# Kernel optimization log

Measured on AMD Instinct MI355X. Metric: run time of the kernel, lower is better.

The kernel has to match this reference:

```python
import jax, jax.numpy as jnp
import numpy as np

N_NODES = 50000
N_EDGES = 800000
IN_F = 128
HID = 128
OUT = 2


def setup_inputs() -> dict:
    key = jax.random.key(0)
    ks = jax.random.split(key, 10)
    x = jax.random.normal(ks[0], (N_NODES, IN_F), dtype=jnp.float32)
    edge_index = jax.random.randint(ks[1], (2, N_EDGES), 0, N_NODES, dtype=jnp.int64)

    def lin(k, fan_in, fan_out):
        s = 1.0 / np.sqrt(fan_in)
        return jax.random.uniform(k, (fan_in, fan_out), jnp.float32, -s, s)

    return {
        "x": x,
        "edge_index": edge_index,
        # SAGEConv1: lin_l applied to mean-aggregated neighbors (with bias),
        # lin_r applied to root features (no bias), PyG convention.
        "W1_l": lin(ks[2], IN_F, HID),
        "W1_r": lin(ks[3], IN_F, HID),
        "b1": jnp.zeros((HID,), jnp.float32),
        "W2_l": lin(ks[4], HID, HID),
        "W2_r": lin(ks[5], HID, HID),
        "b2": jnp.zeros((HID,), jnp.float32),
        "Wfc": lin(ks[6], HID, OUT),
        "bfc": jnp.zeros((OUT,), jnp.float32),
    }


def reference(x, edge_index, W1_l, W1_r, b1, W2_l, W2_r, b2, Wfc, bfc):
    n = x.shape[0]
    src = edge_index[0]  # message source j
    dst = edge_index[1]  # aggregation target i
    # in-degree for mean aggregation (clamp to avoid div-by-zero for isolated nodes)
    deg = jax.ops.segment_sum(jnp.ones_like(dst, dtype=x.dtype), dst, num_segments=n)
    inv_deg = 1.0 / jnp.maximum(deg, 1.0)  # [n]

    def sage_conv(h, Wl, Wr, b):
        # mean over incoming neighbor features, then two linear maps
        agg = jax.ops.segment_sum(h[src], dst, num_segments=n) * inv_deg[:, None]
        return agg @ Wl + h @ Wr + b

    # dropout is identity at inference (training=False)
    h = jax.nn.relu(sage_conv(x, W1_l, W1_r, b1))
    h = jax.nn.relu(sage_conv(h, W2_l, W2_r, b2))
    return h @ Wfc + bfc  # [n, out] logits
```

## Files before the change

### kernel.cpp

```cpp
#include <hip/hip_runtime.h>

#define NN 50000
#define NE 800000
#define NBLK_S ((NE + 255) / 256)
#define DEGCAP 64

#define CVT_BLKS 6250
#define PREP_BLKS 32
#define ZERO_BLKS 50
#define SETUP_GRID (CVT_BLKS + PREP_BLKS + ZERO_BLKS)

typedef short short8 __attribute__((ext_vector_type(8)));
typedef short short4v __attribute__((ext_vector_type(4)));
typedef float f32x4 __attribute__((ext_vector_type(4)));
typedef _Float16 half8v __attribute__((ext_vector_type(8)));

__device__ inline unsigned short f16_bits(float f) {
    _Float16 h = (_Float16)f;
    return __builtin_bit_cast(unsigned short, h);
}

__global__ __launch_bounds__(256) void setup_kernel(const float* __restrict__ x,
                                                    unsigned short* __restrict__ xb,
                                                    const float* __restrict__ W0,
                                                    const float* __restrict__ W1,
                                                    const float* __restrict__ W2,
                                                    const float* __restrict__ W3,
                                                    short* __restrict__ wf,
                                                    int* __restrict__ deg,
                                                    unsigned short* __restrict__ h1b) {
    int b = blockIdx.x;
    if (b < CVT_BLKS) {
        int i = b * 256 + threadIdx.x;
        float4 v = ((const float4*)x)[i];
        short4v r;
        r[0] = (short)f16_bits(v.x);
        r[1] = (short)f16_bits(v.y);
        r[2] = (short)f16_bits(v.z);
        r[3] = (short)f16_bits(v.w);
        ((short4v*)xb)[i] = r;
    } else if (b < CVT_BLKS + PREP_BLKS) {
        int t = (b - CVT_BLKS) * 256 + threadIdx.x;
        int mat = t >> 11;
        const float* W = (mat == 0) ? W0 : (mat == 1) ? W1 : (mat == 2) ? W2 : W3;
        short* out = wf + (size_t)mat * 16384;
        int r = t & 2047;
        int nt = r >> 8;
        int kc = (r >> 6) & 3;
        int lane = r & 63;
        int n = nt * 16 + (lane & 15);
        int kbase = kc * 32 + ((lane >> 4) << 3);
        short8 vh;
#pragma unroll
        for (int j = 0; j < 8; ++j) {
            float w = W[(size_t)(kbase + j) * 128 + n];
            vh[j] = (short)f16_bits(w);
        }
        size_t o = ((size_t)((nt * 4 + kc) * 64 + lane)) * 8;
        *(short8*)(out + o) = vh;
    } else {
        int bl = b - CVT_BLKS - PREP_BLKS;
        int idx = bl * 256 + threadIdx.x;
        if (idx < (NN / 4)) ((int4*)deg)[idx] = make_int4(0, 0, 0, 0);
        if (bl == ZERO_BLKS - 1) {
            int t = threadIdx.x;
            short8 z = {0, 0, 0, 0, 0, 0, 0, 0};
            if (t < 16) *(short8*)(xb + ((size_t)NN << 7) + (t << 3)) = z;
            else if (t < 32) *(short8*)(h1b + ((size_t)NN << 7) + ((t - 16) << 3)) = z;
        }
    }
}

__global__ __launch_bounds__(256) void scatter_kernel(const int* __restrict__ src,
                                                      const int* __restrict__ dst,
                                                      int* __restrict__ deg,
                                                      int* __restrict__ col, int ne) {
    int i = blockIdx.x * 256 + threadIdx.x;
    if (i >= ne) return;
    int d = dst[i];
    int s = src[i];
    int slot = atomicAdd(&deg[d], 1);
    col[((size_t)d << 6) + slot] = s;
}

__global__ __launch_bounds__(256) void agg_kernel(const unsigned short* __restrict__ hb,
                                                  const int* __restrict__ col,
                                                  const int* __restrict__ deg,
                                                  unsigned short* __restrict__ outb, int n) {
    int node = blockIdx.x * 4 + (threadIdx.x >> 6);
    if (node >= n) return;
    int lane = threadIdx.x & 63;
    int slot = lane >> 4, sub = lane & 15;
    int dg = deg[node];
    const unsigned short* base = hb + (sub << 3);
    const int* cp = col + ((size_t)node << 6);
    float acc[8];
#pragma unroll
    for (int j = 0; j < 8; ++j) acc[j] = 0.f;

    for (int e0 = slot; e0 < dg; e0 += 16) {
        int c[4];
#pragma unroll
        for (int j = 0; j < 4; ++j) {
            int e = e0 + 4 * j;
            int cc = cp[e < DEGCAP ? e : 0];
            c[j] = (e < dg) ? cc : NN;
        }
        half8v v[4];
#pragma unroll
        for (int j = 0; j < 4; ++j) v[j] = *(const half8v*)(base + ((size_t)c[j] << 7));
        half8v s = (v[0] + v[1]) + (v[2] + v[3]);
#pragma unroll
        for (int q = 0; q < 8; ++q) acc[q] += (float)s[q];
    }
#pragma unroll
    for (int j = 0; j < 8; ++j) {
        acc[j] += __shfl_xor(acc[j], 16, 64);
        acc[j] += __shfl_xor(acc[j], 32, 64);
    }
    if (slot == 0) {
        float s = 1.0f / (float)(dg > 0 ? dg : 1);
        short8 o;
#pragma unroll
        for (int j = 0; j < 8; ++j) o[j] = (short)f16_bits(acc[j] * s);
        *(short8*)(outb + ((size_t)node << 7) + (sub << 3)) = o;
    }
}

__global__ __launch_bounds__(256) void gemm_mfma(const unsigned short* __restrict__ A0b,
                                                 const unsigned short* __restrict__ A1b,
                                                 const short* __restrict__ Wf0,
                                                 const short* __restrict__ Wf1,
                                                 const float* __restrict__ bias,
                                                 unsigned short* __restrict__ outb,
                                                 const float* __restrict__ Wfc,
                                                 const float* __restrict__ bfc,
                                                 float* __restrict__ fcout,
                                                 int n, int relu) {
    int lane = threadIdx.x & 63;
    int wave = threadIdx.x >> 6;
    int quad = lane >> 4, m16 = lane & 15;
    int row_base = blockIdx.x * 64 + wave * 16;
    int arow = row_base + m16;
    if (arow > n - 1) arow = n - 1;

    const unsigned short* ap0 = A0b + ((size_t)arow << 7) + (quad << 3);
    const unsigned short* ap1 = A1b + ((size_t)arow << 7) + (quad << 3);
    half8v a0[4], a1[4];
#pragma unroll
    for (int kc = 0; kc < 4; ++kc) {
        a0[kc] = *(const half8v*)(ap0 + kc * 32);
        a1[kc] = *(const half8v*)(ap1 + kc * 32);
    }

    f32x4 acc[8];
#pragma unroll
    for (int nt = 0; nt < 8; ++nt) acc[nt] = (f32x4){0.f, 0.f, 0.f, 0.f};

#pragma unroll
    for (int kc = 0; kc < 4; ++kc) {
        const short* wp0 = Wf0 + ((size_t)kc * 64 + lane) * 8;
        const short* wp1 = Wf1 + ((size_t)kc * 64 + lane) * 8;
#pragma unroll
        for (int nt = 0; nt < 8; ++nt) {
            half8v b0 = *(const half8v*)(wp0 + (size_t)nt * 2048);
            half8v b1 = *(const half8v*)(wp1 + (size_t)nt * 2048);
            acc[nt] = __builtin_amdgcn_mfma_f32_16x16x32_f16(a0[kc], b0, acc[nt], 0, 0, 0);
            acc[nt] = __builtin_amdgcn_mfma_f32_16x16x32_f16(a1[kc], b1, acc[nt], 0, 0, 0);
        }
    }

    float bcol[8];
#pragma unroll
    for (int nt = 0; nt < 8; ++nt) bcol[nt] = bias[nt * 16 + m16];

    if (Wfc) {
        float w0[8], w1[8];
#pragma unroll
        for (int nt = 0; nt < 8; ++nt) {
            float2 wv = *(const float2*)(Wfc + 2 * (nt * 16 + m16));
            w0[nt] = wv.x;
            w1[nt] = wv.y;
        }
        float b0 = bfc[0], b1 = bfc[1];
#pragma unroll
        for (int r = 0; r < 4; ++r) {
            float p0 = 0.f, p1 = 0.f;
#pragma unroll
            for (int nt = 0; nt < 8; ++nt) {
                float v = fmaxf(acc[nt][r] + bcol[nt], 0.f);
                p0 += v * w0[nt];
                p1 += v * w1[nt];
            }
#pragma unroll
            for (int off = 1; off < 16; off <<= 1) {
                p0 += __shfl_xor(p0, off, 64);
                p1 += __shfl_xor(p1, off, 64);
            }
            int row = row_base + quad * 4 + r;
            if (m16 == 0 && row < n) {
                float2 o;
                o.x = p0 + b0;
                o.y = p1 + b1;
                *(float2*)(fcout + 2 * (size_t)row) = o;
            }
        }
    } else {
#pragma unroll
        for (int r = 0; r < 4; ++r) {
            int row = row_base + quad * 4 + r;
            if (row >= n) continue;
            unsigned short* opb = outb + ((size_t)row << 7) + m16;
#pragma unroll
            for (int nt = 0; nt < 8; ++nt) {
                float v = acc[nt][r] + bcol[nt];
                if (relu) v = fmaxf(v, 0.f);
                opb[nt * 16] = f16_bits(v);
            }
        }
    }
}

extern "C" void kernel_launch(void* const* d_in, const int* in_sizes, int n_in,
                              void* d_out, int out_size, void* d_ws, size_t ws_size,
                              hipStream_t stream) {
    const float* x   = (const float*)d_in[0];
    const int* edge  = (const int*)d_in[1];
    const float* W1l = (const float*)d_in[2];
    const float* W1r = (const float*)d_in[3];
    const float* b1  = (const float*)d_in[4];
    const float* W2l = (const float*)d_in[5];
    const float* W2r = (const float*)d_in[6];
    const float* b2  = (const float*)d_in[7];
    const float* Wfc = (const float*)d_in[8];
    const float* bfc = (const float*)d_in[9];
    float* out = (float*)d_out;

    const int n = NN, ne = NE;
    const int* src = edge;
    const int* dst = edge + ne;

    char* ws = (char*)d_ws;
    size_t off = 0;
    auto alloc = [&](size_t bytes) -> char* {
        char* p = ws + off;
        off = (off + bytes + 511) & ~(size_t)511;
        return p;
    };
    int* deg         = (int*)alloc((size_t)NN * 4);
    short* wf        = (short*)alloc((size_t)4 * 16384 * 2);
    int* col         = (int*)alloc((size_t)NN * DEGCAP * 4);
    unsigned short* xb   = (unsigned short*)alloc((size_t)(n + 1) * 128 * 2);
    unsigned short* aggb = (unsigned short*)alloc((size_t)n * 128 * 2);
    unsigned short* h1b  = (unsigned short*)alloc((size_t)(n + 1) * 128 * 2);
    (void)ws_size; (void)in_sizes; (void)n_in; (void)out_size;

    setup_kernel<<<SETUP_GRID, 256, 0, stream>>>(x, xb, W1l, W1r, W2l, W2r, wf, deg, h1b);
    scatter_kernel<<<NBLK_S, 256, 0, stream>>>(src, dst, deg, col, ne);

    agg_kernel<<<(n + 3) / 4, 256, 0, stream>>>(xb, col, deg, aggb, n);
    gemm_mfma<<<(n + 63) / 64, 256, 0, stream>>>(aggb, xb, wf, wf + 16384, b1, h1b,
                                                 (const float*)0, (const float*)0, (float*)0, n, 1);
    agg_kernel<<<(n + 3) / 4, 256, 0, stream>>>(h1b, col, deg, aggb, n);
    gemm_mfma<<<(n + 63) / 64, 256, 0, stream>>>(aggb, h1b, wf + 2 * 16384, wf + 3 * 16384, b2,
                                                 (unsigned short*)0, Wfc, bfc, out, n, 1);
}
```

Measured before the change: 230.1 us.

## Partition edge scatter by XCD destination range and store 16-bit neighbor indices

```diff
diff --git a/kernel.cpp b/kernel.cpp
--- a/kernel.cpp
+++ b/kernel.cpp
@@ -2,8 +2,13 @@
 
 #define NN 50000
 #define NE 800000
-#define NBLK_S ((NE + 255) / 256)
 #define DEGCAP 64
+
+#define NXCD 8
+#define NPS ((NN + NXCD - 1) / NXCD)
+#define SEPB 4096
+#define NCHUNK ((NE + SEPB - 1) / SEPB)
+#define SCAT_GRID (NCHUNK * NXCD)
 
 #define CVT_BLKS 6250
 #define PREP_BLKS 32
@@ -74,17 +79,25 @@
 __global__ __launch_bounds__(256) void scatter_kernel(const int* __restrict__ src,
                                                       const int* __restrict__ dst,
                                                       int* __restrict__ deg,
-                                                      int* __restrict__ col, int ne) {
-    int i = blockIdx.x * 256 + threadIdx.x;
-    if (i >= ne) return;
-    int d = dst[i];
-    int s = src[i];
-    int slot = atomicAdd(&deg[d], 1);
-    col[((size_t)d << 6) + slot] = s;
+                                                      unsigned short* __restrict__ col, int ne) {
+    int slot8 = blockIdx.x & 7;
+    int chunk = blockIdx.x >> 3;
+    int lo = slot8 * NPS, hi = lo + NPS;
+    int base = chunk * SEPB;
+    int end = base + SEPB;
+    if (end > ne) end = ne;
+    for (int i = base + threadIdx.x; i < end; i += 256) {
+        int d = dst[i];
+        if (d >= lo && d < hi) {
+            int s = src[i];
+            int sl = atomicAdd(&deg[d], 1);
+            col[((size_t)d << 6) + sl] = (unsigned short)s;
+        }
+    }
 }
 
 __global__ __launch_bounds__(256) void agg_kernel(const unsigned short* __restrict__ hb,
-                                                  const int* __restrict__ col,
+                                                  const unsigned short* __restrict__ col,
                                                   const int* __restrict__ deg,
                                                   unsigned short* __restrict__ outb, int n) {
     int node = blockIdx.x * 4 + (threadIdx.x >> 6);
@@ -93,7 +106,7 @@
     int slot = lane >> 4, sub = lane & 15;
     int dg = deg[node];
     const unsigned short* base = hb + (sub << 3);
-    const int* cp = col + ((size_t)node << 6);
+    const unsigned short* cp = col + ((size_t)node << 6);
     float acc[8];
 #pragma unroll
     for (int j = 0; j < 8; ++j) acc[j] = 0.f;
@@ -247,16 +260,16 @@
         off = (off + bytes + 511) & ~(size_t)511;
         return p;
     };
-    int* deg         = (int*)alloc((size_t)NN * 4);
-    short* wf        = (short*)alloc((size_t)4 * 16384 * 2);
-    int* col         = (int*)alloc((size_t)NN * DEGCAP * 4);
-    unsigned short* xb   = (unsigned short*)alloc((size_t)(n + 1) * 128 * 2);
-    unsigned short* aggb = (unsigned short*)alloc((size_t)n * 128 * 2);
-    unsigned short* h1b  = (unsigned short*)alloc((size_t)(n + 1) * 128 * 2);
+    int* deg              = (int*)alloc((size_t)NN * 4);
+    short* wf             = (short*)alloc((size_t)4 * 16384 * 2);
+    unsigned short* col   = (unsigned short*)alloc((size_t)NN * DEGCAP * 2);
+    unsigned short* xb    = (unsigned short*)alloc((size_t)(n + 1) * 128 * 2);
+    unsigned short* aggb  = (unsigned short*)alloc((size_t)n * 128 * 2);
+    unsigned short* h1b   = (unsigned short*)alloc((size_t)(n + 1) * 128 * 2);
     (void)ws_size; (void)in_sizes; (void)n_in; (void)out_size;
 
     setup_kernel<<<SETUP_GRID, 256, 0, stream>>>(x, xb, W1l, W1r, W2l, W2r, wf, deg, h1b);
-    scatter_kernel<<<NBLK_S, 256, 0, stream>>>(src, dst, deg, col, ne);
+    scatter_kernel<<<SCAT_GRID, 256, 0, stream>>>(src, dst, deg, col, ne);
 
     agg_kernel<<<(n + 3) / 4, 256, 0, stream>>>(xb, col, deg, aggb, n);
     gemm_mfma<<<(n + 63) / 64, 256, 0, stream>>>(aggb, xb, wf, wf + 16384, b1, h1b,
```

After: 212.4 us. 1.08x faster.
